# Kernel tuning notes

Hardware: AMD Instinct MI355X
Metric: run time of the kernel (lower is better)

## Reference

```python
import jax, jax.numpy as jnp
import numpy as np

# dims
B, T, C = 8, 2048, 768          # batch, tokens, n_embed
E, K, H = 8, 2, 3072            # n_experts, top_k, n_mlp_hidden
LOAD = 1.25
CAP = int(LOAD * K * T // E)    # expert_capacity = 640
N_LAYER = 12


def setup_inputs() -> dict:
    key = jax.random.key(0)
    ks = jax.random.split(key, 6)
    s = 0.02
    s_proj = 0.02 * (2 * N_LAYER) ** (-0.5)
    return {
        "x": jax.random.normal(ks[0], (B, T, C), jnp.float32),
        "w_router": (jax.random.normal(ks[1], (C, E), jnp.float32) * s),
        "b_router": jnp.zeros((E,), jnp.float32),
        "w_c_fc": (jax.random.normal(ks[2], (E, C, H), jnp.float32) * s),
        "b_c_fc": jnp.zeros((E, 1, H), jnp.float32),
        "w_gate": (jax.random.normal(ks[3], (E, C, H), jnp.float32) * s),
        "b_gate": jnp.zeros((E, 1, H), jnp.float32),
        "w_c_proj": (jax.random.normal(ks[4], (E, H, C), jnp.float32) * s_proj),
        "b_c_proj": jnp.zeros((E, 1, C), jnp.float32),
    }


def _route(xb, probs):
    """Per-sequence top-k routing + capacity-based scatter dispatch.
    xb: [T, C], probs: [T, E] -> (topk_probs [T,K], pos [T,K], ei [T,K], buf [E,CAP,C])"""
    topk_probs, idx = jax.lax.top_k(probs, K)          # [T, K]
    ei = jnp.swapaxes(idx, 0, 1).ravel()               # [K*T], k-major like original
    oh = jax.nn.one_hot(ei, E, dtype=jnp.int32)        # [K*T, E]
    pos = jnp.cumsum(oh, axis=0) * oh - 1              # running slot per expert
    pos = jnp.max(jnp.swapaxes(pos.reshape(K, T, E), 0, 1), axis=2)  # [T, K]
    ei = jnp.swapaxes(ei.reshape(K, T), 0, 1)          # [T, K]
    xr = jnp.repeat(xb, K, axis=0)                     # [T*K, C], token-major
    # out-of-capacity positions (>= CAP) are dropped by jax scatter semantics,
    # matching the original module.
    buf = jnp.zeros((E, CAP, C), xb.dtype).at[ei.ravel(), pos.ravel()].set(xr)
    return topk_probs, pos, ei, buf


def reference(x, w_router, b_router, w_c_fc, b_c_fc, w_gate, b_gate,
              w_c_proj, b_c_proj):
    gate_logits = jnp.einsum("btc,ce->bte", x, w_router) + b_router
    gate_probs = jax.nn.softmax(gate_logits)
    topk_probs, pos, ei, buf = jax.vmap(_route)(x, gate_probs)  # buf: [B,E,CAP,C]

    # dispatch: expert-major layout (token permutation inside each expert is
    # irrelevant for the per-token expert MLP, so this is equivalent to the
    # original's sharding-oriented reshuffle)
    expert_inputs = jnp.swapaxes(buf, 0, 1).reshape(E, B * CAP, C)

    # grouped-GEMM SwiGLU experts
    h = jnp.einsum("eti,eih->eth", expert_inputs, w_c_fc) + b_c_fc
    g = jnp.einsum("eti,eih->eth", expert_inputs, w_gate) + b_gate
    o = jnp.einsum("eth,eho->eto", jax.nn.silu(h * g), w_c_proj) + b_c_proj

    eo = jnp.swapaxes(o.reshape(E, B, CAP, C), 0, 1)    # [B, E, CAP, C]

    def combine(eo_b, ei_b, pos_b, p_b):
        gathered = eo_b[ei_b, pos_b]                    # [T, K, C]
        return jnp.sum(p_b[..., None] * gathered, axis=1)

    return jax.vmap(combine)(eo, ei, pos, topk_probs)   # [B, T, C]
```

## Files before the change

kernel.cpp:

```cpp
#include <hip/hip_runtime.h>

typedef unsigned short u16;
typedef unsigned int u32;
using u16x4 = __attribute__((ext_vector_type(4))) u16;
using u16x8 = __attribute__((ext_vector_type(8))) u16;
using bf16x8 = __attribute__((ext_vector_type(8))) __bf16;
using f32x4 = __attribute__((ext_vector_type(4))) float;

#define B_ 8
#define T_ 2048
#define C_ 768
#define E_ 8
#define K_ 2
#define H_ 3072
#define CAP_ 640
#define M_ (B_ * CAP_)
#define HC_ 1024
#define NCHUNK_ (H_ / HC_)
#define OVF_MAX_ 32768

__device__ __forceinline__ u16 f2bf(float x) {
  u32 u = __float_as_uint(x);
  u32 r = (u + 0x7FFFu + ((u >> 16) & 1u)) >> 16;
  return (u16)r;
}
__device__ __forceinline__ float bf2f(u16 v) { return __uint_as_float(((u32)v) << 16); }

__device__ __forceinline__ void gl_lds16(const u16* g, u16* l) {
  __builtin_amdgcn_global_load_lds((const __attribute__((address_space(1))) u32*)g,
                                   (__attribute__((address_space(3))) u32*)l, 16, 0, 0);
}
__device__ __forceinline__ bf16x8 ldfrag(const u16* p) {
  return __builtin_bit_cast(bf16x8, *(const u16x8*)p);
}

__global__ void wconv_transpose(const float* __restrict__ in, u16* __restrict__ out,
                                int R, int Cc) {
  __shared__ float tile[32][33];
  const float* inE = in + (size_t)blockIdx.z * R * Cc;
  u16* outE = out + (size_t)blockIdx.z * R * Cc;
  int tx = threadIdx.x & 31, ty = threadIdx.x >> 5;
  int r0 = blockIdx.y * 32, c0 = blockIdx.x * 32;
#pragma unroll
  for (int j = 0; j < 4; j++)
    tile[ty + j * 8][tx] = inE[(size_t)(r0 + ty + j * 8) * Cc + (c0 + tx)];
  __syncthreads();
#pragma unroll
  for (int j = 0; j < 4; j++)
    outE[(size_t)(c0 + ty + j * 8) * R + (r0 + tx)] = f2bf(tile[tx][ty + j * 8]);
}

__global__ void router_kernel(const float* __restrict__ x, const float* __restrict__ wr,
                              const float* __restrict__ br, float* __restrict__ tkp,
                              int* __restrict__ tki) {
  int bt = (blockIdx.x << 2) | (threadIdx.x >> 6);
  int lane = threadIdx.x & 63;
  const float* xr = x + (size_t)bt * C_;
  double acc[E_];
#pragma unroll
  for (int e = 0; e < E_; e++) acc[e] = 0.0;
#pragma unroll
  for (int i = 0; i < C_ / 64; i++) {
    int c = lane + i * 64;
    float xv = xr[c];
    const float* w = wr + c * E_;
#pragma unroll
    for (int e = 0; e < E_; e++) acc[e] += (double)xv * (double)w[e];
  }
#pragma unroll
  for (int off = 32; off > 0; off >>= 1) {
#pragma unroll
    for (int e = 0; e < E_; e++) acc[e] += __shfl_xor(acc[e], off);
  }
  if (lane == 0) {
    double lg[E_];
#pragma unroll
    for (int e = 0; e < E_; e++) lg[e] = acc[e] + (double)br[e];
    int i0 = 0;
#pragma unroll
    for (int e = 1; e < E_; e++) if (lg[e] > lg[i0]) i0 = e;
    int i1 = (i0 == 0) ? 1 : 0;
#pragma unroll
    for (int e = 0; e < E_; e++) if (e != i0 && lg[e] > lg[i1]) i1 = e;
    double mx = lg[i0], s = 0.0, pv[E_];
#pragma unroll
    for (int e = 0; e < E_; e++) { pv[e] = exp(lg[e] - mx); s += pv[e]; }
    tkp[bt * 2 + 0] = (float)(pv[i0] / s);
    tkp[bt * 2 + 1] = (float)(pv[i1] / s);
    tki[bt * 2 + 0] = i0;
    tki[bt * 2 + 1] = i1;
  }
}

__global__ void pos_kernel(const int* __restrict__ tki, int* __restrict__ pos) {
  __shared__ int sc[256][9];
  int b = blockIdx.x;
  int tid = threadIdx.x;
  const int* tib = tki + (size_t)b * T_ * 2;
  int* pb = pos + (size_t)b * T_ * 2;
  int ids[16];
  int cnt[E_];
#pragma unroll
  for (int e = 0; e < E_; e++) cnt[e] = 0;
#pragma unroll
  for (int j = 0; j < 16; j++) {
    int i = tid * 16 + j;
    int k = i >> 11, t = i & (T_ - 1);
    int id = tib[t * 2 + k];
    ids[j] = id;
#pragma unroll
    for (int e = 0; e < E_; e++) cnt[e] += (id == e);
  }
#pragma unroll
  for (int e = 0; e < E_; e++) sc[tid][e] = cnt[e];
  __syncthreads();
  for (int off = 1; off < 256; off <<= 1) {
    int v[E_];
    if (tid >= off) {
#pragma unroll
      for (int e = 0; e < E_; e++) v[e] = sc[tid - off][e];
    }
    __syncthreads();
    if (tid >= off) {
#pragma unroll
      for (int e = 0; e < E_; e++) sc[tid][e] += v[e];
    }
    __syncthreads();
  }
  int base[E_];
#pragma unroll
  for (int e = 0; e < E_; e++) base[e] = (tid > 0) ? sc[tid - 1][e] : 0;
#pragma unroll
  for (int j = 0; j < 16; j++) {
    int i = tid * 16 + j;
    int k = i >> 11, t = i & (T_ - 1);
    int id = ids[j];
    int p = 0;
#pragma unroll
    for (int e = 0; e < E_; e++) p += (id == e) ? base[e] : 0;
    pb[t * 2 + k] = p;
#pragma unroll
    for (int e = 0; e < E_; e++) base[e] += (id == e);
  }
}

__global__ void clear_kernel(int* __restrict__ invt, int* __restrict__ ovfCnt) {
  int i = blockIdx.x * 256 + threadIdx.x;
  invt[i] = -1;
  if (i == 0) *ovfCnt = 0;
}

__global__ void dispatch_kernel(const float* __restrict__ x, const int* __restrict__ tki,
                                const int* __restrict__ pos, u16* __restrict__ Xd,
                                int* __restrict__ invt, int* __restrict__ ovfCnt,
                                int2* __restrict__ ovf) {
  int gw = (blockIdx.x << 2) | (threadIdx.x >> 6);
  int lane = threadIdx.x & 63;
  int bt = gw >> 1;
  int b = bt >> 11;
  int e = tki[gw];
  int p = pos[gw];
  if (p >= CAP_) {
    if (lane == 0) {
      int idx = atomicAdd(ovfCnt, 1);
      if (idx < OVF_MAX_) ovf[idx] = make_int2(bt, gw & 1);
    }
    return;
  }
  size_t row = (size_t)e * M_ + (size_t)b * CAP_ + p;
  if (lane == 0) invt[row] = gw;
  const f32x4* src = (const f32x4*)(x + (size_t)bt * C_);
  u16* dst = Xd + row * C_;
#pragma unroll
  for (int i = 0; i < 3; i++) {
    f32x4 v = src[lane + i * 64];
    u16x4 o;
    o.x = f2bf(v.x); o.y = f2bf(v.y); o.z = f2bf(v.z); o.w = f2bf(v.w);
    *(u16x4*)(dst + (size_t)(lane + i * 64) * 4) = o;
  }
}

__global__ void init_out_kernel(const float* __restrict__ tkp, const int* __restrict__ tki,
                                const float* __restrict__ bp, float* __restrict__ out) {
  int bt = (blockIdx.x << 2) | (threadIdx.x >> 6);
  int lane = threadIdx.x & 63;
  int e0 = tki[bt * 2], e1 = tki[bt * 2 + 1];
  float w0 = tkp[bt * 2], w1 = tkp[bt * 2 + 1];
  const f32x4* b0 = (const f32x4*)(bp + (size_t)e0 * C_);
  const f32x4* b1 = (const f32x4*)(bp + (size_t)e1 * C_);
  f32x4* orow = (f32x4*)(out + (size_t)bt * C_);
#pragma unroll
  for (int i = 0; i < 3; i++) {
    int c = lane + i * 64;
    orow[c] = w0 * b0[c] + w1 * b1[c];
  }
}

__global__ __launch_bounds__(256, 2) void gemm_fc_gate(
    const u16* __restrict__ Xd, const u16* __restrict__ WfcT, const u16* __restrict__ WgT,
    const float* __restrict__ bfc, const float* __restrict__ bg, u16* __restrict__ S,
    int hc) {
  __shared__ __align__(16) u16 Alds[128 * 32];
  __shared__ __align__(16) u16 B1lds[128 * 32];
  __shared__ __align__(16) u16 B2lds[128 * 32];
  int bid = blockIdx.x;
  int e = bid / (40 * (HC_ / 128));
  int t = bid % (40 * (HC_ / 128));
  int tm = t / (HC_ / 128), tn = t % (HC_ / 128);
  int tid = threadIdx.x;
  int lane = tid & 63, wv = tid >> 6;
  int wm = wv & 1, wn = wv >> 1;
  int lr = lane & 15, quad = lane >> 4;

  const u16* XdE = Xd + (size_t)e * M_ * C_;
  const u16* B1E = WfcT + ((size_t)e * H_ + (size_t)hc * HC_) * C_;
  const u16* B2E = WgT + ((size_t)e * H_ + (size_t)hc * HC_) * C_;

  int rhalf = tid >> 2;
  int chunk = tid & 3;
  const u16* gA0 = XdE + (size_t)(tm * 128 + rhalf) * C_ + chunk * 8;
  const u16* gA1 = gA0 + 64 * C_;
  const u16* gB10 = B1E + (size_t)(tn * 128 + rhalf) * C_ + chunk * 8;
  const u16* gB11 = gB10 + 64 * C_;
  const u16* gB20 = B2E + (size_t)(tn * 128 + rhalf) * C_ + chunk * 8;
  const u16* gB21 = gB20 + 64 * C_;
  u16* lA0 = Alds + (wv * 16) * 32;
  u16* lA1 = Alds + (64 + wv * 16) * 32;
  u16* lB10 = B1lds + (wv * 16) * 32;
  u16* lB11 = B1lds + (64 + wv * 16) * 32;
  u16* lB20 = B2lds + (wv * 16) * 32;
  u16* lB21 = B2lds + (64 + wv * 16) * 32;

  f32x4 acc1[4][4], acc2[4][4];
#pragma unroll
  for (int i = 0; i < 4; i++)
#pragma unroll
    for (int j = 0; j < 4; j++) {
      acc1[i][j] = (f32x4){0.f, 0.f, 0.f, 0.f};
      acc2[i][j] = (f32x4){0.f, 0.f, 0.f, 0.f};
    }

  for (int kt = 0; kt < C_ / 32; kt++) {
    int ko = kt * 32;
    __syncthreads();
    gl_lds16(gA0 + ko, lA0);
    gl_lds16(gA1 + ko, lA1);
    gl_lds16(gB10 + ko, lB10);
    gl_lds16(gB11 + ko, lB11);
    gl_lds16(gB20 + ko, lB20);
    gl_lds16(gB21 + ko, lB21);
    __syncthreads();
    bf16x8 af[4], b1f[4], b2f[4];
#pragma unroll
    for (int i = 0; i < 4; i++) {
      af[i] = ldfrag(Alds + (wm * 64 + i * 16 + lr) * 32 + quad * 8);
      b1f[i] = ldfrag(B1lds + (wn * 64 + i * 16 + lr) * 32 + quad * 8);
      b2f[i] = ldfrag(B2lds + (wn * 64 + i * 16 + lr) * 32 + quad * 8);
    }
#pragma unroll
    for (int i = 0; i < 4; i++)
#pragma unroll
      for (int j = 0; j < 4; j++) {
        acc1[i][j] = __builtin_amdgcn_mfma_f32_16x16x32_bf16(af[i], b1f[j], acc1[i][j], 0, 0, 0);
        acc2[i][j] = __builtin_amdgcn_mfma_f32_16x16x32_bf16(af[i], b2f[j], acc2[i][j], 0, 0, 0);
      }
  }

  u16* Se = S + (size_t)e * M_ * HC_;
  const float* bfcE = bfc + (size_t)e * H_ + (size_t)hc * HC_;
  const float* bgE = bg + (size_t)e * H_ + (size_t)hc * HC_;
  int col0 = tn * 128 + wn * 64 + lr;
  int row0 = tm * 128 + wm * 64 + quad * 4;
#pragma unroll
  for (int j = 0; j < 4; j++) {
    int col = col0 + j * 16;
    float bf_ = bfcE[col], bg_ = bgE[col];
#pragma unroll
    for (int i = 0; i < 4; i++) {
      int row = row0 + i * 16;
#pragma unroll
      for (int r = 0; r < 4; r++) {
        float h = acc1[i][j][r] + bf_;
        float g = acc2[i][j][r] + bg_;
        float z = h * g;
        float sv = z / (1.f + __expf(-z));
        Se[(size_t)(row + r) * HC_ + col] = f2bf(sv);
      }
    }
  }
}

__global__ __launch_bounds__(256, 2) void gemm_proj_scatter(
    const u16* __restrict__ S, const u16* __restrict__ WpT,
    const int* __restrict__ invt, const float* __restrict__ tkp,
    const int* __restrict__ tki, const int* __restrict__ ovfCnt,
    const int2* __restrict__ ovf, float* __restrict__ out, int hc) {
  __shared__ __align__(16) u16 Alds[128 * 32];
  __shared__ __align__(16) u16 Blds[128 * 32];
  int bid = blockIdx.x;
  int e = bid / (40 * 6);
  int t = bid % (40 * 6);
  int tm = t / 6, tn = t % 6;
  int tid = threadIdx.x;
  int lane = tid & 63, wv = tid >> 6;
  int wm = wv & 1, wn = wv >> 1;
  int lr = lane & 15, quad = lane >> 4;

  const u16* SE = S + (size_t)e * M_ * HC_;
  const u16* BE = WpT + (size_t)e * C_ * H_ + (size_t)hc * HC_;

  int rhalf = tid >> 2;
  int chunk = tid & 3;
  const u16* gA0 = SE + (size_t)(tm * 128 + rhalf) * HC_ + chunk * 8;
  const u16* gA1 = gA0 + 64 * HC_;
  const u16* gB0 = BE + (size_t)(tn * 128 + rhalf) * H_ + chunk * 8;
  const u16* gB1 = gB0 + 64 * H_;
  u16* lA0 = Alds + (wv * 16) * 32;
  u16* lA1 = Alds + (64 + wv * 16) * 32;
  u16* lB0 = Blds + (wv * 16) * 32;
  u16* lB1 = Blds + (64 + wv * 16) * 32;

  f32x4 acc[4][4];
#pragma unroll
  for (int i = 0; i < 4; i++)
#pragma unroll
    for (int j = 0; j < 4; j++) acc[i][j] = (f32x4){0.f, 0.f, 0.f, 0.f};

  for (int kt = 0; kt < HC_ / 32; kt++) {
    int ko = kt * 32;
    __syncthreads();
    gl_lds16(gA0 + ko, lA0);
    gl_lds16(gA1 + ko, lA1);
    gl_lds16(gB0 + ko, lB0);
    gl_lds16(gB1 + ko, lB1);
    __syncthreads();
    bf16x8 af[4], bf[4];
#pragma unroll
    for (int i = 0; i < 4; i++) {
      af[i] = ldfrag(Alds + (wm * 64 + i * 16 + lr) * 32 + quad * 8);
      bf[i] = ldfrag(Blds + (wn * 64 + i * 16 + lr) * 32 + quad * 8);
    }
#pragma unroll
    for (int i = 0; i < 4; i++)
#pragma unroll
      for (int j = 0; j < 4; j++)
        acc[i][j] = __builtin_amdgcn_mfma_f32_16x16x32_bf16(af[i], bf[j], acc[i][j], 0, 0, 0);
  }

  int col0 = tn * 128 + wn * 64 + lr;
  int row0 = tm * 128 + wm * 64 + quad * 4;
  const int* invtE = invt + e * M_;
#pragma unroll
  for (int i = 0; i < 4; i++) {
#pragma unroll
    for (int r = 0; r < 4; r++) {
      int re = row0 + i * 16 + r;
      int g = invtE[re];
      if (g >= 0) {
        float w = tkp[g];
        float* orow = out + (size_t)(g >> 1) * C_;
#pragma unroll
        for (int j = 0; j < 4; j++)
          atomicAdd(orow + col0 + j * 16, w * acc[i][j][r]);
      }
    }
  }
  if (wm == 1 && quad == 3 && (tm % 5) == 4) {
    int b = tm / 5;
    int nov = *ovfCnt;
    if (nov > OVF_MAX_) nov = OVF_MAX_;
    for (int o = 0; o < nov; o++) {
      int2 en = ovf[o];
      int gw2 = en.x * 2 + en.y;
      if (tki[gw2] == e && (en.x >> 11) == b) {
        float w = tkp[gw2];
        float* orow = out + (size_t)en.x * C_;
#pragma unroll
        for (int j = 0; j < 4; j++)
          atomicAdd(orow + col0 + j * 16, w * acc[3][j][3]);
      }
    }
  }
}

extern "C" void kernel_launch(void* const* d_in, const int* in_sizes, int n_in,
                              void* d_out, int out_size, void* d_ws, size_t ws_size,
                              hipStream_t stream) {
  (void)in_sizes; (void)n_in; (void)out_size; (void)ws_size;
  const float* x = (const float*)d_in[0];
  const float* w_router = (const float*)d_in[1];
  const float* b_router = (const float*)d_in[2];
  const float* w_c_fc = (const float*)d_in[3];
  const float* b_c_fc = (const float*)d_in[4];
  const float* w_gate = (const float*)d_in[5];
  const float* b_gate = (const float*)d_in[6];
  const float* w_c_proj = (const float*)d_in[7];
  const float* b_c_proj = (const float*)d_in[8];
  float* out = (float*)d_out;

  char* p = (char*)d_ws;
  auto alloc = [&](size_t n) { char* r = p; p += (n + 255) & ~(size_t)255; return r; };
  const size_t WN = (size_t)E_ * C_ * H_;
  u16* WfcT = (u16*)alloc(WN * 2);
  u16* WgT = (u16*)alloc(WN * 2);
  u16* WpT = (u16*)alloc(WN * 2);
  u16* Xd = (u16*)alloc((size_t)E_ * M_ * C_ * 2);
  float* tkp = (float*)alloc((size_t)B_ * T_ * 2 * 4);
  int* tki = (int*)alloc((size_t)B_ * T_ * 2 * 4);
  int* pos = (int*)alloc((size_t)B_ * T_ * 2 * 4);
  int* invt = (int*)alloc((size_t)E_ * M_ * 4);
  int* ovfCnt = (int*)alloc(4);
  int2* ovf = (int2*)alloc((size_t)OVF_MAX_ * 8);
  u16* S = (u16*)alloc((size_t)E_ * M_ * HC_ * 2);

  dim3 blk(256);
  wconv_transpose<<<dim3(H_ / 32, C_ / 32, E_), blk, 0, stream>>>(w_c_fc, WfcT, C_, H_);
  wconv_transpose<<<dim3(H_ / 32, C_ / 32, E_), blk, 0, stream>>>(w_gate, WgT, C_, H_);
  wconv_transpose<<<dim3(C_ / 32, H_ / 32, E_), blk, 0, stream>>>(w_c_proj, WpT, H_, C_);

  router_kernel<<<dim3(B_ * T_ / 4), blk, 0, stream>>>(x, w_router, b_router, tkp, tki);
  pos_kernel<<<dim3(B_), blk, 0, stream>>>(tki, pos);
  clear_kernel<<<dim3(E_ * M_ / 256), blk, 0, stream>>>(invt, ovfCnt);
  dispatch_kernel<<<dim3(B_ * T_ * K_ / 4), blk, 0, stream>>>(x, tki, pos, Xd, invt, ovfCnt, ovf);
  init_out_kernel<<<dim3(B_ * T_ / 4), blk, 0, stream>>>(tkp, tki, b_c_proj, out);

  for (int hc = 0; hc < NCHUNK_; hc++) {
    gemm_fc_gate<<<dim3(E_ * 40 * (HC_ / 128)), blk, 0, stream>>>(
        Xd, WfcT, WgT, b_c_fc, b_gate, S, hc);
    gemm_proj_scatter<<<dim3(E_ * 40 * 6), blk, 0, stream>>>(
        S, WpT, invt, tkp, tki, ovfCnt, ovf, out, hc);
  }
}
```

Baseline: 1.294 ms.

## Double-buffer LDS with XOR swizzle and XCD-aware block remap in expert GEMMs

Both expert GEMM kernels now prefetch the next K-slice into a second LDS buffer while MFMAs run on the current one, which cuts the loop from two barriers to one. Rows are XOR-swizzled in 16-byte chunks on both the global-to-LDS write and the fragment read, to reduce LDS bank conflicts. Block IDs are remapped so consecutive tiles land on the same XCD for L2 reuse, and the proj kernel's launch-bounds occupancy hint is raised from 2 to 3. The cost is double the LDS use per block and possible extra register pressure from the higher occupancy target.

```diff
diff --git a/kernel.cpp b/kernel.cpp
--- a/kernel.cpp
+++ b/kernel.cpp
@@ -200,10 +200,10 @@
     const u16* __restrict__ Xd, const u16* __restrict__ WfcT, const u16* __restrict__ WgT,
     const float* __restrict__ bfc, const float* __restrict__ bg, u16* __restrict__ S,
     int hc) {
-  __shared__ __align__(16) u16 Alds[128 * 32];
-  __shared__ __align__(16) u16 B1lds[128 * 32];
-  __shared__ __align__(16) u16 B2lds[128 * 32];
-  int bid = blockIdx.x;
+  __shared__ __align__(16) u16 lds[2][3][128 * 32];
+  const int NWG = E_ * 40 * (HC_ / 128);
+  int bid0 = blockIdx.x;
+  int bid = (bid0 & 7) * (NWG >> 3) + (bid0 >> 3);
   int e = bid / (40 * (HC_ / 128));
   int t = bid % (40 * (HC_ / 128));
   int tm = t / (HC_ / 128), tn = t % (HC_ / 128);
@@ -218,18 +218,15 @@
 
   int rhalf = tid >> 2;
   int chunk = tid & 3;
-  const u16* gA0 = XdE + (size_t)(tm * 128 + rhalf) * C_ + chunk * 8;
+  int swzc = chunk ^ ((rhalf >> 1) & 3);
+  const u16* gA0 = XdE + (size_t)(tm * 128 + rhalf) * C_ + swzc * 8;
   const u16* gA1 = gA0 + 64 * C_;
-  const u16* gB10 = B1E + (size_t)(tn * 128 + rhalf) * C_ + chunk * 8;
+  const u16* gB10 = B1E + (size_t)(tn * 128 + rhalf) * C_ + swzc * 8;
   const u16* gB11 = gB10 + 64 * C_;
-  const u16* gB20 = B2E + (size_t)(tn * 128 + rhalf) * C_ + chunk * 8;
+  const u16* gB20 = B2E + (size_t)(tn * 128 + rhalf) * C_ + swzc * 8;
   const u16* gB21 = gB20 + 64 * C_;
-  u16* lA0 = Alds + (wv * 16) * 32;
-  u16* lA1 = Alds + (64 + wv * 16) * 32;
-  u16* lB10 = B1lds + (wv * 16) * 32;
-  u16* lB11 = B1lds + (64 + wv * 16) * 32;
-  u16* lB20 = B2lds + (wv * 16) * 32;
-  u16* lB21 = B2lds + (64 + wv * 16) * 32;
+  int ldsW0 = (wv * 16) * 32;
+  int ldsW1 = (64 + wv * 16) * 32;
 
   f32x4 acc1[4][4], acc2[4][4];
 #pragma unroll
@@ -240,22 +237,37 @@
       acc2[i][j] = (f32x4){0.f, 0.f, 0.f, 0.f};
     }
 
-  for (int kt = 0; kt < C_ / 32; kt++) {
-    int ko = kt * 32;
-    __syncthreads();
-    gl_lds16(gA0 + ko, lA0);
-    gl_lds16(gA1 + ko, lA1);
-    gl_lds16(gB10 + ko, lB10);
-    gl_lds16(gB11 + ko, lB11);
-    gl_lds16(gB20 + ko, lB20);
-    gl_lds16(gB21 + ko, lB21);
-    __syncthreads();
+  const int NK = C_ / 32;
+  int rs = (quad ^ ((lr >> 1) & 3)) * 8;
+
+  {
+    gl_lds16(gA0, &lds[0][0][0] + ldsW0);
+    gl_lds16(gA1, &lds[0][0][0] + ldsW1);
+    gl_lds16(gB10, &lds[0][1][0] + ldsW0);
+    gl_lds16(gB11, &lds[0][1][0] + ldsW1);
+    gl_lds16(gB20, &lds[0][2][0] + ldsW0);
+    gl_lds16(gB21, &lds[0][2][0] + ldsW1);
+  }
+  __syncthreads();
+
+  int cur = 0;
+  for (int kt = 0; kt < NK; kt++) {
+    if (kt + 1 < NK) {
+      int ko = (kt + 1) * 32;
+      int nb = cur ^ 1;
+      gl_lds16(gA0 + ko, &lds[nb][0][0] + ldsW0);
+      gl_lds16(gA1 + ko, &lds[nb][0][0] + ldsW1);
+      gl_lds16(gB10 + ko, &lds[nb][1][0] + ldsW0);
+      gl_lds16(gB11 + ko, &lds[nb][1][0] + ldsW1);
+      gl_lds16(gB20 + ko, &lds[nb][2][0] + ldsW0);
+      gl_lds16(gB21 + ko, &lds[nb][2][0] + ldsW1);
+    }
     bf16x8 af[4], b1f[4], b2f[4];
 #pragma unroll
     for (int i = 0; i < 4; i++) {
-      af[i] = ldfrag(Alds + (wm * 64 + i * 16 + lr) * 32 + quad * 8);
-      b1f[i] = ldfrag(B1lds + (wn * 64 + i * 16 + lr) * 32 + quad * 8);
-      b2f[i] = ldfrag(B2lds + (wn * 64 + i * 16 + lr) * 32 + quad * 8);
+      af[i] = ldfrag(&lds[cur][0][0] + (wm * 64 + i * 16 + lr) * 32 + rs);
+      b1f[i] = ldfrag(&lds[cur][1][0] + (wn * 64 + i * 16 + lr) * 32 + rs);
+      b2f[i] = ldfrag(&lds[cur][2][0] + (wn * 64 + i * 16 + lr) * 32 + rs);
     }
 #pragma unroll
     for (int i = 0; i < 4; i++)
@@ -264,6 +276,8 @@
         acc1[i][j] = __builtin_amdgcn_mfma_f32_16x16x32_bf16(af[i], b1f[j], acc1[i][j], 0, 0, 0);
         acc2[i][j] = __builtin_amdgcn_mfma_f32_16x16x32_bf16(af[i], b2f[j], acc2[i][j], 0, 0, 0);
       }
+    __syncthreads();
+    cur ^= 1;
   }
 
   u16* Se = S + (size_t)e * M_ * HC_;
@@ -290,14 +304,15 @@
   }
 }
 
-__global__ __launch_bounds__(256, 2) void gemm_proj_scatter(
+__global__ __launch_bounds__(256, 3) void gemm_proj_scatter(
     const u16* __restrict__ S, const u16* __restrict__ WpT,
     const int* __restrict__ invt, const float* __restrict__ tkp,
     const int* __restrict__ tki, const int* __restrict__ ovfCnt,
     const int2* __restrict__ ovf, float* __restrict__ out, int hc) {
-  __shared__ __align__(16) u16 Alds[128 * 32];
-  __shared__ __align__(16) u16 Blds[128 * 32];
-  int bid = blockIdx.x;
+  __shared__ __align__(16) u16 lds[2][2][128 * 32];
+  const int NWG = E_ * 40 * 6;
+  int bid0 = blockIdx.x;
+  int bid = (bid0 & 7) * (NWG >> 3) + (bid0 >> 3);
   int e = bid / (40 * 6);
   int t = bid % (40 * 6);
   int tm = t / 6, tn = t % 6;
@@ -311,14 +326,13 @@
 
   int rhalf = tid >> 2;
   int chunk = tid & 3;
-  const u16* gA0 = SE + (size_t)(tm * 128 + rhalf) * HC_ + chunk * 8;
+  int swzc = chunk ^ ((rhalf >> 1) & 3);
+  const u16* gA0 = SE + (size_t)(tm * 128 + rhalf) * HC_ + swzc * 8;
   const u16* gA1 = gA0 + 64 * HC_;
-  const u16* gB0 = BE + (size_t)(tn * 128 + rhalf) * H_ + chunk * 8;
+  const u16* gB0 = BE + (size_t)(tn * 128 + rhalf) * H_ + swzc * 8;
   const u16* gB1 = gB0 + 64 * H_;
-  u16* lA0 = Alds + (wv * 16) * 32;
-  u16* lA1 = Alds + (64 + wv * 16) * 32;
-  u16* lB0 = Blds + (wv * 16) * 32;
-  u16* lB1 = Blds + (64 + wv * 16) * 32;
+  int ldsW0 = (wv * 16) * 32;
+  int ldsW1 = (64 + wv * 16) * 32;
 
   f32x4 acc[4][4];
 #pragma unroll
@@ -326,25 +340,40 @@
 #pragma unroll
     for (int j = 0; j < 4; j++) acc[i][j] = (f32x4){0.f, 0.f, 0.f, 0.f};
 
-  for (int kt = 0; kt < HC_ / 32; kt++) {
-    int ko = kt * 32;
-    __syncthreads();
-    gl_lds16(gA0 + ko, lA0);
-    gl_lds16(gA1 + ko, lA1);
-    gl_lds16(gB0 + ko, lB0);
-    gl_lds16(gB1 + ko, lB1);
-    __syncthreads();
+  const int NK = HC_ / 32;
+  int rs = (quad ^ ((lr >> 1) & 3)) * 8;
+
+  {
+    gl_lds16(gA0, &lds[0][0][0] + ldsW0);
+    gl_lds16(gA1, &lds[0][0][0] + ldsW1);
+    gl_lds16(gB0, &lds[0][1][0] + ldsW0);
+    gl_lds16(gB1, &lds[0][1][0] + ldsW1);
+  }
+  __syncthreads();
+
+  int cur = 0;
+  for (int kt = 0; kt < NK; kt++) {
+    if (kt + 1 < NK) {
+      int ko = (kt + 1) * 32;
+      int nb = cur ^ 1;
+      gl_lds16(gA0 + ko, &lds[nb][0][0] + ldsW0);
+      gl_lds16(gA1 + ko, &lds[nb][0][0] + ldsW1);
+      gl_lds16(gB0 + ko, &lds[nb][1][0] + ldsW0);
+      gl_lds16(gB1 + ko, &lds[nb][1][0] + ldsW1);
+    }
     bf16x8 af[4], bf[4];
 #pragma unroll
     for (int i = 0; i < 4; i++) {
-      af[i] = ldfrag(Alds + (wm * 64 + i * 16 + lr) * 32 + quad * 8);
-      bf[i] = ldfrag(Blds + (wn * 64 + i * 16 + lr) * 32 + quad * 8);
+      af[i] = ldfrag(&lds[cur][0][0] + (wm * 64 + i * 16 + lr) * 32 + rs);
+      bf[i] = ldfrag(&lds[cur][1][0] + (wn * 64 + i * 16 + lr) * 32 + rs);
     }
 #pragma unroll
     for (int i = 0; i < 4; i++)
 #pragma unroll
       for (int j = 0; j < 4; j++)
         acc[i][j] = __builtin_amdgcn_mfma_f32_16x16x32_bf16(af[i], bf[j], acc[i][j], 0, 0, 0);
+    __syncthreads();
+    cur ^= 1;
   }
 
   int col0 = tn * 128 + wn * 64 + lr;
```

Result: faster. 1.150 ms (-11.1%).
